# Optimization experiments

Hardware: AMD Instinct MI355X
Metric: run time of the kernel (lower is better)

The kernel has to match this reference:

```python
import jax, jax.numpy as jnp
import numpy as np

EPS = 1e-06


def setup_inputs() -> dict:
    key = jax.random.key(0)
    kq, kk, kv = jax.random.split(key, 3)
    B, H, T, P = 2, 8, 1024, 64
    Q = jax.random.normal(kq, (B, H, T, P), dtype=jnp.float32)
    K = jax.random.normal(kk, (B, H, T, P), dtype=jnp.float32)
    V = jax.random.normal(kv, (B, H, T, P), dtype=jnp.float32)
    return {"Q": Q, "K": K, "V": V}


def _scan_attention(Q, K, V):
    Q_feat = jnp.exp(Q)                                  # (B,H,T,P)
    K_feat = jnp.exp(K)                                  # (B,H,T,P)
    m0 = jnp.log(K_feat)                                 # (B,H,T,P)
    N0 = jnp.einsum('bhtp,bhtn->bhtpn', V, K_feat)       # (B,H,T,P,P) matrix state
    D0 = K_feat                                          # (B,H,T,P)

    def combine(x, y):
        m_x, N_x, D_x = x
        m_y, N_y, D_y = y
        m_new = jnp.maximum(m_x, m_y)
        scale_x = jnp.exp(m_x - m_new)
        scale_y = jnp.exp(m_y - m_new)
        N_new = N_x * scale_x[..., None] + N_y * scale_y[..., None]
        D_new = D_x * scale_x + D_y * scale_y
        return (m_new, N_new, D_new)

    m_cum, num_cum, denom_cum = jax.lax.associative_scan(combine, (m0, N0, D0), axis=2)

    Y_num = jnp.einsum('bhtp,bhtpq->bhtq', Q_feat, num_cum)   # (B,H,T,P)
    Y_den = jnp.einsum('bhtp,bhtp->bht', Q_feat, denom_cum)   # (B,H,T)
    Y = Y_num / (Y_den[..., None] + EPS)
    B, H, T, P = Q.shape
    return Y.transpose(0, 2, 1, 3).reshape(B, T, H * P)


def reference(Q, K, V):
    return _scan_attention(Q, K, V)
```

## Files before the change

kernel.cpp:

```cpp
#include <hip/hip_runtime.h>
#include <hip/hip_bf16.h>

#define TDIM 1024
#define PDIM 64
#define BHN  16
#define NCH  64
#define CHS  16

typedef __bf16 bf16_t;
typedef bf16_t bf16x8 __attribute__((ext_vector_type(8)));
typedef float  floatx4 __attribute__((ext_vector_type(4)));

__device__ __forceinline__ floatx4 mfma16(bf16x8 a, bf16x8 b, floatx4 c) {
    return __builtin_amdgcn_mfma_f32_16x16x32_bf16(a, b, c, 0, 0, 0);
}

__global__ __launch_bounds__(64) void stats_kernel(
        const float* __restrict__ K,
        float* __restrict__ cmax, float* __restrict__ csum) {
    int bh = blockIdx.x >> 6;
    int c  = blockIdx.x & 63;
    int p  = threadIdx.x;
    const float* Kb = K + (size_t)bh * TDIM * PDIM + (size_t)c * CHS * PDIM + p;
    float k[CHS];
#pragma unroll
    for (int i = 0; i < CHS; ++i) k[i] = Kb[i * PDIM];
    float m = -INFINITY, s = 0.f;
#pragma unroll
    for (int i = 0; i < CHS; ++i) {
        m = fmaxf(m, k[i]);
        float e = __expf(k[i]);
        s += e * e;
    }
    cmax[(bh * NCH + c) * PDIM + p] = m;
    csum[(bh * NCH + c) * PDIM + p] = s;
}

__global__ __launch_bounds__(64) void feat_kernel(
        const float* __restrict__ Q, const float* __restrict__ K,
        const float* __restrict__ V,
        const float* __restrict__ cmax, const float* __restrict__ csum,
        bf16_t* __restrict__ W, bf16_t* __restrict__ U,
        bf16_t* __restrict__ Kft, float* __restrict__ den) {
    int bh = blockIdx.x >> 6;
    int c  = blockIdx.x & 63;
    int p  = threadIdx.x;
    size_t base = (size_t)bh * TDIM * PDIM;
    int t0 = c * CHS;

    float m = -INFINITY, s = 0.f;
#pragma unroll 8
    for (int cc = 0; cc < c; ++cc) {
        m = fmaxf(m, cmax[(bh * NCH + cc) * PDIM + p]);
        s += csum[(bh * NCH + cc) * PDIM + p];
    }

    float kq[CHS], qq_[CHS], vv[CHS];
#pragma unroll
    for (int i = 0; i < CHS; ++i) {
        kq[i]  = K[base + (size_t)(t0 + i) * PDIM + p];
        qq_[i] = Q[base + (size_t)(t0 + i) * PDIM + p];
        vv[i]  = V[base + (size_t)(t0 + i) * PDIM + p];
    }

    __shared__ bf16_t ek_t[CHS][PDIM + 4];
    __shared__ float  dt[CHS][PDIM + 1];

#pragma unroll
    for (int i = 0; i < CHS; ++i) {
        int t = t0 + i;
        m = fmaxf(m, kq[i]);
        float ek = __expf(kq[i]);
        s += ek * ek;
        float w = __expf(qq_[i] - m);
        W[base + (size_t)t * PDIM + p] = (bf16_t)w;
        U[base + (size_t)t * PDIM + p] = (bf16_t)(vv[i] * ek);
        ek_t[i][p] = (bf16_t)ek;
        dt[i][p] = w * s;
    }
    __syncthreads();

    {
        int tl = p >> 2, g = p & 3;
        float d = 0.f;
#pragma unroll
        for (int i = 0; i < 16; ++i) d += dt[tl][i * 4 + g];
        d += __shfl_xor(d, 1);
        d += __shfl_xor(d, 2);
        if (g == 0) den[bh * TDIM + t0 + tl] = d;
    }

    {
        int hi = p >> 4, tl = p & 15;
#pragma unroll
        for (int it = 0; it < 16; ++it) {
            int q = it * 4 + hi;
            Kft[((size_t)bh * PDIM + q) * TDIM + t0 + tl] = ek_t[tl][q];
        }
    }
}

__global__ __launch_bounds__(512) void attn_kernel(
        const bf16_t* __restrict__ W, const bf16_t* __restrict__ U,
        const bf16_t* __restrict__ Kft, const float* __restrict__ den,
        float* __restrict__ out) {
    int bh  = blockIdx.x & 15;
    int i   = blockIdx.x >> 4;
    int tid = threadIdx.x;
    int wave = tid >> 6, lane = tid & 63;
    int lq = lane & 15, qd = lane >> 4;
    int sub = wave & 3;
    int par = wave >> 2;
    int b = bh >> 3, h = bh & 7;

    __shared__ bf16_t Wt[64][72];
    __shared__ bf16_t Ut[2][64][72];
    __shared__ bf16_t Kt[2][64][72];
    __shared__ __align__(16) char ctyraw[8 * 16 * 72 * 2];
    __shared__ float denb[64];
    bf16_t (*Ct)[16][72]  = (bf16_t (*)[16][72])ctyraw;
    float  (*Yred)[16][68] = (float (*)[16][68])ctyraw;

    size_t base = (size_t)bh * TDIM * PDIM;
    size_t kftb = (size_t)bh * PDIM * TDIM;
    int row = tid >> 3, c8 = (tid & 7) << 3;

    int4 wfrag = *(const int4*)(W + base + (size_t)(i * 64 + row) * PDIM + c8);
    int4 pu0 = *(const int4*)(U + base + (size_t)(0 * 64 + row) * PDIM + c8);
    int4 pk0 = *(const int4*)(Kft + kftb + (size_t)row * TDIM + 0 * 64 + c8);
    int4 pu1 = *(const int4*)(U + base + (size_t)(1 * 64 + row) * PDIM + c8);
    int4 pk1 = *(const int4*)(Kft + kftb + (size_t)row * TDIM + 1 * 64 + c8);
    *(int4*)&Wt[row][c8] = wfrag;
    if (tid < 64) denb[tid] = den[bh * TDIM + i * 64 + tid];
    __syncthreads();

    bf16x8 a0 = *(const bf16x8*)&Wt[sub * 16 + lq][qd * 8];
    bf16x8 a1 = *(const bf16x8*)&Wt[sub * 16 + lq][32 + qd * 8];

    floatx4 acc[4];
#pragma unroll
    for (int j = 0; j < 4; ++j) acc[j] = (floatx4){0.f, 0.f, 0.f, 0.f};

    int niter = (i >> 1) + 1;
    for (int kt2 = 0; kt2 < niter; ++kt2) {
        __syncthreads();
        *(int4*)&Ut[0][row][c8] = pu0;
        *(int4*)&Kt[0][row][c8] = pk0;
        *(int4*)&Ut[1][row][c8] = pu1;
        *(int4*)&Kt[1][row][c8] = pk1;
        if (kt2 + 1 < niter) {
            int ktn = 2 * kt2 + 2;
            int ktn1 = ktn + 1 > 15 ? 15 : ktn + 1;
            pu0 = *(const int4*)(U + base + (size_t)(ktn * 64 + row) * PDIM + c8);
            pk0 = *(const int4*)(Kft + kftb + (size_t)row * TDIM + ktn * 64 + c8);
            pu1 = *(const int4*)(U + base + (size_t)(ktn1 * 64 + row) * PDIM + c8);
            pk1 = *(const int4*)(Kft + kftb + (size_t)row * TDIM + ktn1 * 64 + c8);
        }
        __syncthreads();

        int kt = 2 * kt2 + par;
        if (kt <= i) {
            floatx4 cc[4];
#pragma unroll
            for (int j = 0; j < 4; ++j) {
                bf16x8 b0 = *(const bf16x8*)&Ut[par][j * 16 + lq][qd * 8];
                bf16x8 b1 = *(const bf16x8*)&Ut[par][j * 16 + lq][32 + qd * 8];
                floatx4 t = (floatx4){0.f, 0.f, 0.f, 0.f};
                t = mfma16(a0, b0, t);
                t = mfma16(a1, b1, t);
                cc[j] = t;
            }
            int trow0 = i * 64 + sub * 16;
#pragma unroll
            for (int j = 0; j < 4; ++j) {
#pragma unroll
                for (int r = 0; r < 4; ++r) {
                    float v = cc[j][r];
                    if (kt == i && (kt * 64 + j * 16 + lq) > (trow0 + qd * 4 + r))
                        v = 0.f;
                    Ct[wave][qd * 4 + r][j * 16 + lq] = (bf16_t)v;
                }
            }
            bf16x8 ca0 = *(const bf16x8*)&Ct[wave][lq][qd * 8];
            bf16x8 ca1 = *(const bf16x8*)&Ct[wave][lq][32 + qd * 8];
#pragma unroll
            for (int j = 0; j < 4; ++j) {
                bf16x8 kb0 = *(const bf16x8*)&Kt[par][j * 16 + lq][qd * 8];
                bf16x8 kb1 = *(const bf16x8*)&Kt[par][j * 16 + lq][32 + qd * 8];
                acc[j] = mfma16(ca0, kb0, acc[j]);
                acc[j] = mfma16(ca1, kb1, acc[j]);
            }
        }
    }

    __syncthreads();
    if (par == 1) {
#pragma unroll
        for (int j = 0; j < 4; ++j)
#pragma unroll
            for (int r = 0; r < 4; ++r)
                Yred[sub][qd * 4 + r][j * 16 + lq] = acc[j][r];
    }
    __syncthreads();
    if (par == 0) {
#pragma unroll
        for (int j = 0; j < 4; ++j) {
#pragma unroll
            for (int r = 0; r < 4; ++r) {
                int trow_l = sub * 16 + qd * 4 + r;
                int tg = i * 64 + trow_l;
                float y = acc[j][r] + Yred[sub][qd * 4 + r][j * 16 + lq];
                y = y / (denb[trow_l] + 1e-6f);
                out[((size_t)b * TDIM + tg) * (8 * PDIM) + h * PDIM + j * 16 + lq] = y;
            }
        }
    }
}

extern "C" void kernel_launch(void* const* d_in, const int* in_sizes, int n_in,
                              void* d_out, int out_size, void* d_ws, size_t ws_size,
                              hipStream_t stream) {
    const float* Q = (const float*)d_in[0];
    const float* K = (const float*)d_in[1];
    const float* V = (const float*)d_in[2];
    float* out = (float*)d_out;

    bf16_t* Wf   = (bf16_t*)d_ws;
    bf16_t* Uf   = Wf + (size_t)BHN * TDIM * PDIM;
    bf16_t* Kft  = Uf + (size_t)BHN * TDIM * PDIM;
    float*  den  = (float*)(Kft + (size_t)BHN * TDIM * PDIM);
    float*  cmax = den + (size_t)BHN * TDIM;
    float*  csum = cmax + (size_t)BHN * NCH * PDIM;

    stats_kernel<<<BHN * NCH, 64, 0, stream>>>(K, cmax, csum);
    feat_kernel<<<BHN * NCH, 64, 0, stream>>>(Q, K, V, cmax, csum, Wf, Uf, Kft, den);
    attn_kernel<<<256, 512, 0, stream>>>(Wf, Uf, Kft, den, out);
}
```

Measured before the change: 85.29 us.

## Fuse chunk stats into feature kernel by recomputing prefix max/sum directly

Removes the separate stats kernel and its cmax/csum buffers. Each feature block now recomputes the running max and sum of exp(K)^2 by scanning all prior rows of K itself, using four independent accumulators. This saves a kernel launch and the dependency between kernels, but costs quadratic redundant reads and exps of K, up to 1008 rows per block. Block order is also changed to interleave heads.

```diff
diff --git a/kernel.cpp b/kernel.cpp
--- a/kernel.cpp
+++ b/kernel.cpp
@@ -15,45 +15,17 @@
     return __builtin_amdgcn_mfma_f32_16x16x32_bf16(a, b, c, 0, 0, 0);
 }
 
-__global__ __launch_bounds__(64) void stats_kernel(
-        const float* __restrict__ K,
-        float* __restrict__ cmax, float* __restrict__ csum) {
-    int bh = blockIdx.x >> 6;
-    int c  = blockIdx.x & 63;
-    int p  = threadIdx.x;
-    const float* Kb = K + (size_t)bh * TDIM * PDIM + (size_t)c * CHS * PDIM + p;
-    float k[CHS];
-#pragma unroll
-    for (int i = 0; i < CHS; ++i) k[i] = Kb[i * PDIM];
-    float m = -INFINITY, s = 0.f;
-#pragma unroll
-    for (int i = 0; i < CHS; ++i) {
-        m = fmaxf(m, k[i]);
-        float e = __expf(k[i]);
-        s += e * e;
-    }
-    cmax[(bh * NCH + c) * PDIM + p] = m;
-    csum[(bh * NCH + c) * PDIM + p] = s;
-}
-
-__global__ __launch_bounds__(64) void feat_kernel(
+__global__ __launch_bounds__(64) void scanfeat_kernel(
         const float* __restrict__ Q, const float* __restrict__ K,
         const float* __restrict__ V,
-        const float* __restrict__ cmax, const float* __restrict__ csum,
         bf16_t* __restrict__ W, bf16_t* __restrict__ U,
         bf16_t* __restrict__ Kft, float* __restrict__ den) {
-    int bh = blockIdx.x >> 6;
-    int c  = blockIdx.x & 63;
+    int g  = blockIdx.x;
+    int bh = g & 15;
+    int c  = g >> 4;
     int p  = threadIdx.x;
     size_t base = (size_t)bh * TDIM * PDIM;
     int t0 = c * CHS;
-
-    float m = -INFINITY, s = 0.f;
-#pragma unroll 8
-    for (int cc = 0; cc < c; ++cc) {
-        m = fmaxf(m, cmax[(bh * NCH + cc) * PDIM + p]);
-        s += csum[(bh * NCH + cc) * PDIM + p];
-    }
 
     float kq[CHS], qq_[CHS], vv[CHS];
 #pragma unroll
@@ -63,31 +35,51 @@
         vv[i]  = V[base + (size_t)(t0 + i) * PDIM + p];
     }
 
+    const float* Kb = K + base + p;
+    float m0 = -INFINITY, m1 = -INFINITY, m2 = -INFINITY, m3 = -INFINITY;
+    float s0 = 0.f, s1 = 0.f, s2 = 0.f, s3 = 0.f;
+    int nrows = t0;
+    int t = 0;
+#pragma unroll 2
+    for (; t + 4 <= nrows; t += 4) {
+        float k0 = Kb[(size_t)(t + 0) * PDIM];
+        float k1 = Kb[(size_t)(t + 1) * PDIM];
+        float k2 = Kb[(size_t)(t + 2) * PDIM];
+        float k3 = Kb[(size_t)(t + 3) * PDIM];
+        m0 = fmaxf(m0, k0); m1 = fmaxf(m1, k1);
+        m2 = fmaxf(m2, k2); m3 = fmaxf(m3, k3);
+        float e0 = __expf(k0), e1 = __expf(k1);
+        float e2 = __expf(k2), e3 = __expf(k3);
+        s0 += e0 * e0; s1 += e1 * e1; s2 += e2 * e2; s3 += e3 * e3;
+    }
+    float m = fmaxf(fmaxf(m0, m1), fmaxf(m2, m3));
+    float s = (s0 + s1) + (s2 + s3);
+
     __shared__ bf16_t ek_t[CHS][PDIM + 4];
     __shared__ float  dt[CHS][PDIM + 1];
 
 #pragma unroll
     for (int i = 0; i < CHS; ++i) {
-        int t = t0 + i;
+        int tg = t0 + i;
         m = fmaxf(m, kq[i]);
         float ek = __expf(kq[i]);
         s += ek * ek;
         float w = __expf(qq_[i] - m);
-        W[base + (size_t)t * PDIM + p] = (bf16_t)w;
-        U[base + (size_t)t * PDIM + p] = (bf16_t)(vv[i] * ek);
+        W[base + (size_t)tg * PDIM + p] = (bf16_t)w;
+        U[base + (size_t)tg * PDIM + p] = (bf16_t)(vv[i] * ek);
         ek_t[i][p] = (bf16_t)ek;
         dt[i][p] = w * s;
     }
     __syncthreads();
 
     {
-        int tl = p >> 2, g = p & 3;
+        int tl = p >> 2, gg = p & 3;
         float d = 0.f;
 #pragma unroll
-        for (int i = 0; i < 16; ++i) d += dt[tl][i * 4 + g];
+        for (int i = 0; i < 16; ++i) d += dt[tl][i * 4 + gg];
         d += __shfl_xor(d, 1);
         d += __shfl_xor(d, 2);
-        if (g == 0) den[bh * TDIM + t0 + tl] = d;
+        if (gg == 0) den[bh * TDIM + t0 + tl] = d;
     }
 
     {
@@ -229,10 +221,7 @@
     bf16_t* Uf   = Wf + (size_t)BHN * TDIM * PDIM;
     bf16_t* Kft  = Uf + (size_t)BHN * TDIM * PDIM;
     float*  den  = (float*)(Kft + (size_t)BHN * TDIM * PDIM);
-    float*  cmax = den + (size_t)BHN * TDIM;
-    float*  csum = cmax + (size_t)BHN * NCH * PDIM;
-
-    stats_kernel<<<BHN * NCH, 64, 0, stream>>>(K, cmax, csum);
-    feat_kernel<<<BHN * NCH, 64, 0, stream>>>(Q, K, V, cmax, csum, Wf, Uf, Kft, den);
+
+    scanfeat_kernel<<<BHN * NCH, 64, 0, stream>>>(Q, K, V, Wf, Uf, Kft, den);
     attn_kernel<<<256, 512, 0, stream>>>(Wf, Uf, Kft, den, out);
 }
```

Measured after the change: 101.8 us. 1.19x slower.
